# Performance work log

Measured on AMD Instinct MI355X. Metric: run time of the kernel, lower is better.

Reference implementation:

```python
import jax, jax.numpy as jnp
import numpy as np

EPS = 1e-6


def setup_inputs() -> dict:
    key = jax.random.key(0)
    k1, k2, k3, k4 = jax.random.split(key, 4)
    dim = 3072
    seq = 8192
    x = jax.random.normal(k1, (1, seq, dim), dtype=jnp.float32)
    emb = jax.random.normal(k2, (1, dim), dtype=jnp.float32)
    W = jax.random.normal(k3, (3 * dim, dim), dtype=jnp.float32) * 0.02
    b = jax.random.normal(k4, (3 * dim,), dtype=jnp.float32) * 0.02
    return {"x": x, "emb": emb, "W": W, "b": b}


def reference(x, emb, W, b):
    # SiLU + linear (dequantized-equivalent of int4 AWQ GEMV): [1,dim]x[dim,3dim] -> [1,3dim]
    e = jnp.dot(jax.nn.silu(emb), W.T) + b
    # Interleaved unpack: reshape (1, dim, 3) then unbind last axis (matches torch code)
    e3 = e.reshape(1, -1, 3)
    shift_msa = e3[..., 0]  # [1, dim]
    scale_msa = e3[..., 1]
    gate_msa = e3[..., 2]
    # LayerNorm over last dim, no affine, eps=1e-6
    mean = jnp.mean(x, axis=-1, keepdims=True)
    var = jnp.mean(jnp.square(x - mean), axis=-1, keepdims=True)
    xn = (x - mean) * jax.lax.rsqrt(var + EPS)
    out = xn * scale_msa[:, None] + shift_msa[:, None]
    return (out, gate_msa)
```

## Files before the change

kernel.cpp:

```cpp
#include <hip/hip_runtime.h>
#include <math.h>

#define DIM 3072
#define SEQ 8192
#define NROWS (3 * DIM)

__device__ __forceinline__ float silu_f(float v) {
    return v / (1.0f + __expf(-v));
}

__global__ __launch_bounds__(256, 4) void gemv3_kernel(
    const float* __restrict__ emb, const float* __restrict__ W,
    const float* __restrict__ b, float* __restrict__ shift,
    float* __restrict__ scale, float* __restrict__ gate)
{
    __shared__ float s[DIM];
    const int t = threadIdx.x;
    const float4* emb4 = (const float4*)emb;
    float4* s4 = (float4*)s;

    #pragma unroll
    for (int k = 0; k < 3; ++k) {
        int i = t + k * 256;
        float4 v = emb4[i];
        v.x = silu_f(v.x); v.y = silu_f(v.y);
        v.z = silu_f(v.z); v.w = silu_f(v.w);
        s4[i] = v;
    }
    __syncthreads();

    const int wid = t >> 6;
    const int lane = t & 63;
    const int row = blockIdx.x * 4 + wid;
    const float4* w4 = (const float4*)(W + (size_t)row * DIM);

    float acc = 0.f;
    #pragma unroll
    for (int k = 0; k < 12; ++k) {
        int i = lane + 64 * k;
        float4 w = w4[i];
        float4 v = s4[i];
        acc += w.x * v.x + w.y * v.y + w.z * v.z + w.w * v.w;
    }

    #pragma unroll
    for (int off = 32; off > 0; off >>= 1)
        acc += __shfl_xor(acc, off, 64);

    if (lane == 0) {
        float e = acc + b[row];
        int i = row / 3;
        int r = row - 3 * i;
        if (r == 0)      shift[i] = e;
        else if (r == 1) scale[i] = e;
        else             gate[i]  = e;
    }
}

__global__ __launch_bounds__(256, 4) void ln_affine_kernel(
    const float* __restrict__ x, const float* __restrict__ shift,
    const float* __restrict__ scale, float* __restrict__ out)
{
    const int t = threadIdx.x;
    const int wid = t >> 6;
    const int lane = t & 63;
    const int row = blockIdx.x * 4 + wid;
    const float4* x4 = (const float4*)(x + (size_t)row * DIM);
    float4* o4 = (float4*)(out + (size_t)row * DIM);
    const float4* sc4 = (const float4*)scale;
    const float4* sh4 = (const float4*)shift;

    float4 v[12];
    float sum = 0.f, sq = 0.f;
    #pragma unroll
    for (int k = 0; k < 12; ++k) {
        v[k] = x4[lane + 64 * k];
        sum += v[k].x + v[k].y + v[k].z + v[k].w;
        sq  += v[k].x * v[k].x + v[k].y * v[k].y + v[k].z * v[k].z + v[k].w * v[k].w;
    }

    #pragma unroll
    for (int off = 32; off > 0; off >>= 1) {
        sum += __shfl_xor(sum, off, 64);
        sq  += __shfl_xor(sq,  off, 64);
    }

    const float mean = sum * (1.0f / DIM);
    const float rstd = rsqrtf(sq * (1.0f / DIM) - mean * mean + 1e-6f);

    #pragma unroll
    for (int k = 0; k < 12; ++k) {
        int i = lane + 64 * k;
        float4 sc = sc4[i];
        float4 sh = sh4[i];
        float4 r;
        r.x = (v[k].x - mean) * rstd * sc.x + sh.x;
        r.y = (v[k].y - mean) * rstd * sc.y + sh.y;
        r.z = (v[k].z - mean) * rstd * sc.z + sh.z;
        r.w = (v[k].w - mean) * rstd * sc.w + sh.w;
        o4[i] = r;
    }
}

extern "C" void kernel_launch(void* const* d_in, const int* in_sizes, int n_in,
                              void* d_out, int out_size, void* d_ws, size_t ws_size,
                              hipStream_t stream) {
    const float* x   = (const float*)d_in[0];
    const float* emb = (const float*)d_in[1];
    const float* W   = (const float*)d_in[2];
    const float* b   = (const float*)d_in[3];
    float* out  = (float*)d_out;
    float* gate = out + (size_t)SEQ * DIM;
    float* shift = (float*)d_ws;
    float* scale = shift + DIM;

    gemv3_kernel<<<NROWS / 4, 256, 0, stream>>>(emb, W, b, shift, scale, gate);
    ln_affine_kernel<<<SEQ / 4, 256, 0, stream>>>(x, shift, scale, out);
}
```

Before: 67.39 us.

## Process two rows per wavefront in LayerNorm and stage scale/shift in LDS

```diff
diff --git a/kernel.cpp b/kernel.cpp
--- a/kernel.cpp
+++ b/kernel.cpp
@@ -37,9 +37,8 @@
     float acc = 0.f;
     #pragma unroll
     for (int k = 0; k < 12; ++k) {
-        int i = lane + 64 * k;
-        float4 w = w4[i];
-        float4 v = s4[i];
+        float4 w = w4[lane + 64 * k];
+        float4 v = s4[lane + 64 * k];
         acc += w.x * v.x + w.y * v.y + w.z * v.z + w.w * v.w;
     }
 
@@ -61,44 +60,93 @@
     const float* __restrict__ x, const float* __restrict__ shift,
     const float* __restrict__ scale, float* __restrict__ out)
 {
+    __shared__ float s_sc[DIM];
+    __shared__ float s_sh[DIM];
     const int t = threadIdx.x;
     const int wid = t >> 6;
     const int lane = t & 63;
-    const int row = blockIdx.x * 4 + wid;
-    const float4* x4 = (const float4*)(x + (size_t)row * DIM);
-    float4* o4 = (float4*)(out + (size_t)row * DIM);
-    const float4* sc4 = (const float4*)scale;
-    const float4* sh4 = (const float4*)shift;
 
-    float4 v[12];
-    float sum = 0.f, sq = 0.f;
+    {
+        const float4* scg = (const float4*)scale;
+        const float4* shg = (const float4*)shift;
+        float4* ssc = (float4*)s_sc;
+        float4* ssh = (float4*)s_sh;
+        #pragma unroll
+        for (int k = 0; k < 3; ++k) {
+            int i = t + k * 256;
+            ssc[i] = scg[i];
+            ssh[i] = shg[i];
+        }
+    }
+    __syncthreads();
+    const float4* lsc = (const float4*)s_sc;
+    const float4* lsh = (const float4*)s_sh;
+
+    const int row0 = (blockIdx.x * 4 + wid) * 2;
+    const int row1 = row0 + 1;
+    const float4* xA = (const float4*)(x + (size_t)row0 * DIM);
+    const float4* xB = (const float4*)(x + (size_t)row1 * DIM);
+    float4* oA = (float4*)(out + (size_t)row0 * DIM);
+    float4* oB = (float4*)(out + (size_t)row1 * DIM);
+
+    float4 v0[12];
+    float sum0 = 0.f, sq0 = 0.f;
     #pragma unroll
     for (int k = 0; k < 12; ++k) {
-        v[k] = x4[lane + 64 * k];
-        sum += v[k].x + v[k].y + v[k].z + v[k].w;
-        sq  += v[k].x * v[k].x + v[k].y * v[k].y + v[k].z * v[k].z + v[k].w * v[k].w;
+        v0[k] = xA[lane + 64 * k];
+        sum0 += v0[k].x + v0[k].y + v0[k].z + v0[k].w;
+        sq0  += v0[k].x * v0[k].x + v0[k].y * v0[k].y + v0[k].z * v0[k].z + v0[k].w * v0[k].w;
+    }
+
+    float4 v1[12];
+    float sum1 = 0.f, sq1 = 0.f;
+    #pragma unroll
+    for (int k = 0; k < 12; ++k) {
+        v1[k] = xB[lane + 64 * k];
+        sum1 += v1[k].x + v1[k].y + v1[k].z + v1[k].w;
+        sq1  += v1[k].x * v1[k].x + v1[k].y * v1[k].y + v1[k].z * v1[k].z + v1[k].w * v1[k].w;
     }
 
     #pragma unroll
     for (int off = 32; off > 0; off >>= 1) {
-        sum += __shfl_xor(sum, off, 64);
-        sq  += __shfl_xor(sq,  off, 64);
+        sum0 += __shfl_xor(sum0, off, 64);
+        sq0  += __shfl_xor(sq0,  off, 64);
     }
-
-    const float mean = sum * (1.0f / DIM);
-    const float rstd = rsqrtf(sq * (1.0f / DIM) - mean * mean + 1e-6f);
+    const float mean0 = sum0 * (1.0f / DIM);
+    const float rstd0 = rsqrtf(sq0 * (1.0f / DIM) - mean0 * mean0 + 1e-6f);
 
     #pragma unroll
     for (int k = 0; k < 12; ++k) {
         int i = lane + 64 * k;
-        float4 sc = sc4[i];
-        float4 sh = sh4[i];
+        float4 sc = lsc[i];
+        float4 sh = lsh[i];
         float4 r;
-        r.x = (v[k].x - mean) * rstd * sc.x + sh.x;
-        r.y = (v[k].y - mean) * rstd * sc.y + sh.y;
-        r.z = (v[k].z - mean) * rstd * sc.z + sh.z;
-        r.w = (v[k].w - mean) * rstd * sc.w + sh.w;
-        o4[i] = r;
+        r.x = (v0[k].x - mean0) * rstd0 * sc.x + sh.x;
+        r.y = (v0[k].y - mean0) * rstd0 * sc.y + sh.y;
+        r.z = (v0[k].z - mean0) * rstd0 * sc.z + sh.z;
+        r.w = (v0[k].w - mean0) * rstd0 * sc.w + sh.w;
+        oA[i] = r;
+    }
+
+    #pragma unroll
+    for (int off = 32; off > 0; off >>= 1) {
+        sum1 += __shfl_xor(sum1, off, 64);
+        sq1  += __shfl_xor(sq1,  off, 64);
+    }
+    const float mean1 = sum1 * (1.0f / DIM);
+    const float rstd1 = rsqrtf(sq1 * (1.0f / DIM) - mean1 * mean1 + 1e-6f);
+
+    #pragma unroll
+    for (int k = 0; k < 12; ++k) {
+        int i = lane + 64 * k;
+        float4 sc = lsc[i];
+        float4 sh = lsh[i];
+        float4 r;
+        r.x = (v1[k].x - mean1) * rstd1 * sc.x + sh.x;
+        r.y = (v1[k].y - mean1) * rstd1 * sc.y + sh.y;
+        r.z = (v1[k].z - mean1) * rstd1 * sc.z + sh.z;
+        r.w = (v1[k].w - mean1) * rstd1 * sc.w + sh.w;
+        oB[i] = r;
     }
 }
 
@@ -109,11 +157,11 @@
     const float* emb = (const float*)d_in[1];
     const float* W   = (const float*)d_in[2];
     const float* b   = (const float*)d_in[3];
-    float* out  = (float*)d_out;
-    float* gate = out + (size_t)SEQ * DIM;
+    float* out   = (float*)d_out;
+    float* gate  = out + (size_t)SEQ * DIM;
     float* shift = (float*)d_ws;
     float* scale = shift + DIM;
 
     gemv3_kernel<<<NROWS / 4, 256, 0, stream>>>(emb, W, b, shift, scale, gate);
-    ln_affine_kernel<<<SEQ / 4, 256, 0, stream>>>(x, shift, scale, out);
+    ln_affine_kernel<<<SEQ / 8, 256, 0, stream>>>(x, shift, scale, out);
 }
```

Result: no change. 68.09 us (+1.0%).

## Split LayerNorm into separate stats and apply kernels

Applied to the files above, without the earlier changes.

```diff
diff --git a/kernel.cpp b/kernel.cpp
--- a/kernel.cpp
+++ b/kernel.cpp
@@ -37,9 +37,8 @@
     float acc = 0.f;
     #pragma unroll
     for (int k = 0; k < 12; ++k) {
-        int i = lane + 64 * k;
-        float4 w = w4[i];
-        float4 v = s4[i];
+        float4 w = w4[lane + 64 * k];
+        float4 v = s4[lane + 64 * k];
         acc += w.x * v.x + w.y * v.y + w.z * v.z + w.w * v.w;
     }
 
@@ -57,26 +56,21 @@
     }
 }
 
-__global__ __launch_bounds__(256, 4) void ln_affine_kernel(
-    const float* __restrict__ x, const float* __restrict__ shift,
-    const float* __restrict__ scale, float* __restrict__ out)
+__global__ __launch_bounds__(256, 4) void ln_stats_kernel(
+    const float* __restrict__ x, float2* __restrict__ stats)
 {
     const int t = threadIdx.x;
     const int wid = t >> 6;
     const int lane = t & 63;
     const int row = blockIdx.x * 4 + wid;
     const float4* x4 = (const float4*)(x + (size_t)row * DIM);
-    float4* o4 = (float4*)(out + (size_t)row * DIM);
-    const float4* sc4 = (const float4*)scale;
-    const float4* sh4 = (const float4*)shift;
 
-    float4 v[12];
     float sum = 0.f, sq = 0.f;
     #pragma unroll
     for (int k = 0; k < 12; ++k) {
-        v[k] = x4[lane + 64 * k];
-        sum += v[k].x + v[k].y + v[k].z + v[k].w;
-        sq  += v[k].x * v[k].x + v[k].y * v[k].y + v[k].z * v[k].z + v[k].w * v[k].w;
+        float4 v = x4[lane + 64 * k];
+        sum += v.x + v.y + v.z + v.w;
+        sq  += v.x * v.x + v.y * v.y + v.z * v.z + v.w * v.w;
     }
 
     #pragma unroll
@@ -85,19 +79,38 @@
         sq  += __shfl_xor(sq,  off, 64);
     }
 
-    const float mean = sum * (1.0f / DIM);
-    const float rstd = rsqrtf(sq * (1.0f / DIM) - mean * mean + 1e-6f);
+    if (lane == 0) {
+        float mean = sum * (1.0f / DIM);
+        float rstd = rsqrtf(sq * (1.0f / DIM) - mean * mean + 1e-6f);
+        stats[row] = make_float2(mean, rstd);
+    }
+}
+
+__global__ __launch_bounds__(256, 4) void ln_apply_kernel(
+    const float* __restrict__ x, const float2* __restrict__ stats,
+    const float* __restrict__ shift, const float* __restrict__ scale,
+    float* __restrict__ out)
+{
+    const int row = blockIdx.x;
+    const int t = threadIdx.x;
+    const float2 ms = stats[row];
+    const float mean = ms.x, rstd = ms.y;
+    const float4* x4 = (const float4*)(x + (size_t)row * DIM);
+    float4* o4 = (float4*)(out + (size_t)row * DIM);
+    const float4* sc4 = (const float4*)scale;
+    const float4* sh4 = (const float4*)shift;
 
     #pragma unroll
-    for (int k = 0; k < 12; ++k) {
-        int i = lane + 64 * k;
+    for (int k = 0; k < 3; ++k) {
+        int i = t + k * 256;
+        float4 v = x4[i];
         float4 sc = sc4[i];
         float4 sh = sh4[i];
         float4 r;
-        r.x = (v[k].x - mean) * rstd * sc.x + sh.x;
-        r.y = (v[k].y - mean) * rstd * sc.y + sh.y;
-        r.z = (v[k].z - mean) * rstd * sc.z + sh.z;
-        r.w = (v[k].w - mean) * rstd * sc.w + sh.w;
+        r.x = (v.x - mean) * rstd * sc.x + sh.x;
+        r.y = (v.y - mean) * rstd * sc.y + sh.y;
+        r.z = (v.z - mean) * rstd * sc.z + sh.z;
+        r.w = (v.w - mean) * rstd * sc.w + sh.w;
         o4[i] = r;
     }
 }
@@ -109,11 +122,13 @@
     const float* emb = (const float*)d_in[1];
     const float* W   = (const float*)d_in[2];
     const float* b   = (const float*)d_in[3];
-    float* out  = (float*)d_out;
-    float* gate = out + (size_t)SEQ * DIM;
+    float* out   = (float*)d_out;
+    float* gate  = out + (size_t)SEQ * DIM;
     float* shift = (float*)d_ws;
     float* scale = shift + DIM;
+    float2* stats = (float2*)(scale + DIM);
 
     gemv3_kernel<<<NROWS / 4, 256, 0, stream>>>(emb, W, b, shift, scale, gate);
-    ln_affine_kernel<<<SEQ / 4, 256, 0, stream>>>(x, shift, scale, out);
+    ln_stats_kernel<<<SEQ / 4, 256, 0, stream>>>(x, stats);
+    ln_apply_kernel<<<SEQ, 256, 0, stream>>>(x, stats, shift, scale, out);
 }
```

Measured after the change: 76.06 us. 1.13x slower.
